# Performance work log

Measured on AMD Instinct MI355X. Metric: run time of the kernel, lower is better.

Reference implementation:

```python
import jax, jax.numpy as jnp
import numpy as np
import math

EMBED = 768
HEADS = 12
DK = EMBED // HEADS
FFN = 3072
NQ = 8
B, S = 4, 2048


def _layernorm(x, g, b, eps=1e-5):
    mu = jnp.mean(x, axis=-1, keepdims=True)
    var = jnp.var(x, axis=-1, keepdims=True)
    return (x - mu) * jax.lax.rsqrt(var + eps) * g + b


def setup_inputs() -> dict:
    key = jax.random.key(0)
    ks = jax.random.split(key, 16)
    std = 0.02
    inp = {
        "x": jax.random.normal(ks[0], (B, S, EMBED), dtype=jnp.float32),
        "mask": jnp.ones((B, S), dtype=jnp.int32),
        # attention projections (torch Linear: W [out, in])
        "wq": jax.random.normal(ks[1], (EMBED, EMBED), jnp.float32) * std,
        "bq": jnp.zeros((EMBED,), jnp.float32),
        "wk": jax.random.normal(ks[2], (EMBED, EMBED), jnp.float32) * std,
        "bk": jnp.zeros((EMBED,), jnp.float32),
        "wv": jax.random.normal(ks[3], (EMBED, EMBED), jnp.float32) * std,
        "bv": jnp.zeros((EMBED,), jnp.float32),
        "wo": jax.random.normal(ks[4], (EMBED, EMBED), jnp.float32) * std,
        "bo": jnp.zeros((EMBED,), jnp.float32),
        # layernorms
        "g1": jnp.ones((EMBED,), jnp.float32),
        "be1": jnp.zeros((EMBED,), jnp.float32),
        "g2": jnp.ones((EMBED,), jnp.float32),
        "be2": jnp.zeros((EMBED,), jnp.float32),
        # quantum FFN: trainable RY angles + two linears
        "theta": jax.random.normal(ks[5], (NQ,), jnp.float32) * 0.1,
        "w1": jax.random.normal(ks[6], (FFN, NQ), jnp.float32) * std,
        "b1": jnp.zeros((FFN,), jnp.float32),
        "w2": jax.random.normal(ks[7], (EMBED, FFN), jnp.float32) * std,
        "b2": jnp.zeros((EMBED,), jnp.float32),
    }
    return inp


def _block(x, mask, wq, bq, wk, bk, wv, bv, wo, bo, g1, be1, g2, be2,
           theta, w1, b1, w2, b2):
    b, s, _ = x.shape
    # --- multi-head attention (dropout = identity at eval) ---
    q = (x @ wq.T + bq).reshape(b, s, HEADS, DK)
    k = (x @ wk.T + bk).reshape(b, s, HEADS, DK)
    v = (x @ wv.T + bv).reshape(b, s, HEADS, DK)
    scores = jnp.einsum("bqhd,bkhd->bhqk", q, k) / math.sqrt(DK)
    scores = jnp.where(mask[:, None, None, :] == 0, -1e9, scores)
    attn = jax.nn.softmax(scores, axis=-1)
    ctx = jnp.einsum("bhqk,bkhd->bqhd", attn, v).reshape(b, s, EMBED)
    attn_out = ctx @ wo.T + bo
    x = _layernorm(x + attn_out, g1, be1)
    # --- quantum FFN: RY(x_i) then RY(theta_i) on |0>, <Z> = cos(x_i+theta_i)
    # (product state, no entanglement -> exact closed form, fully batched)
    meas = jnp.cos(x[..., :NQ] + theta)            # [b, s, NQ]
    h = jax.nn.relu(meas @ w1.T + b1)              # [b, s, FFN]
    ffn_out = h @ w2.T + b2                        # [b, s, EMBED]
    return _layernorm(x + ffn_out, g2, be2)


def reference(x, mask, wq, bq, wk, bk, wv, bv, wo, bo, g1, be1, g2, be2,
              theta, w1, b1, w2, b2):
    return _block(x, mask, wq, bq, wk, bk, wv, bv, wo, bo,
                  g1, be1, g2, be2, theta, w1, b1, w2, b2)
```

## Files before the change

kernel.cpp:

```cpp
#include <hip/hip_runtime.h>
#include <hip/hip_bf16.h>


typedef __bf16 bf16_t;
typedef bf16_t bf16x4 __attribute__((ext_vector_type(4)));
typedef bf16_t bf16x8 __attribute__((ext_vector_type(8)));
typedef float floatx4 __attribute__((ext_vector_type(4)));

#define LOG2E 1.44269504088896f

__device__ __forceinline__ void gload16(const bf16_t* g, bf16_t* l) {
    __builtin_amdgcn_global_load_lds(
        (const __attribute__((address_space(1))) unsigned int*)g,
        (__attribute__((address_space(3))) unsigned int*)l,
        16, 0, 0);
}

__device__ __forceinline__ int swz(int row, int col) {
    return row * 64 + (col ^ ((row & 7) << 3));
}

__global__ __launch_bounds__(256)
void prep(const float* __restrict__ x,
          const float* __restrict__ wq, const float* __restrict__ wk,
          const float* __restrict__ wv, const float* __restrict__ wo,
          const float* __restrict__ w2,
          const float* __restrict__ bq, const float* __restrict__ bk,
          const float* __restrict__ bv,
          bf16_t* __restrict__ xb, bf16_t* __restrict__ wqkv,
          bf16_t* __restrict__ wob, bf16_t* __restrict__ w2b,
          float* __restrict__ bqkv)
{
    const int seg = blockIdx.y;
    const int idx = blockIdx.x * 256 + threadIdx.x;
    if (seg == 0) {
        if (idx >= 1572864) return;
        const float4 f = ((const float4*)x)[idx];
        bf16x4 o = {(bf16_t)f.x, (bf16_t)f.y, (bf16_t)f.z, (bf16_t)f.w};
        ((bf16x4*)xb)[idx] = o;
    } else if (seg == 1) {
        if (idx >= 442368) return;
        const int e = idx * 4;
        float4 f = (e < 589824) ? ((const float4*)wq)[idx]
                 : (e < 1179648) ? ((const float4*)wk)[idx - 147456]
                                 : ((const float4*)wv)[idx - 294912];
        if (e < 589824) { f.x *= 0.125f; f.y *= 0.125f; f.z *= 0.125f; f.w *= 0.125f; }
        bf16x4 o = {(bf16_t)f.x, (bf16_t)f.y, (bf16_t)f.z, (bf16_t)f.w};
        ((bf16x4*)wqkv)[idx] = o;
    } else if (seg == 2) {
        if (idx >= 147456) return;
        const float4 f = ((const float4*)wo)[idx];
        bf16x4 o = {(bf16_t)f.x, (bf16_t)f.y, (bf16_t)f.z, (bf16_t)f.w};
        ((bf16x4*)wob)[idx] = o;
    } else if (seg == 3) {
        if (idx >= 589824) return;
        const float4 f = ((const float4*)w2)[idx];
        bf16x4 o = {(bf16_t)f.x, (bf16_t)f.y, (bf16_t)f.z, (bf16_t)f.w};
        ((bf16x4*)w2b)[idx] = o;
    } else {
        if (idx >= 576) return;
        const int e = idx * 4;
        float4 f = (e < 768) ? ((const float4*)bq)[idx]
                 : (e < 1536) ? ((const float4*)bk)[idx - 192]
                              : ((const float4*)bv)[idx - 384];
        if (e < 768) { f.x *= 0.125f; f.y *= 0.125f; f.z *= 0.125f; f.w *= 0.125f; }
        ((float4*)bqkv)[idx] = f;
    }
}

template<typename TC>
__global__ __launch_bounds__(256)
void gemm_bb(const bf16_t* __restrict__ A, const bf16_t* __restrict__ W,
             const float* __restrict__ bias, TC* __restrict__ C,
             int kPer, int lda, int ldw, int ldc, int splitStride)
{
    __shared__ __align__(16) bf16_t As[2][4096];
    __shared__ __align__(16) bf16_t Bs[2][4096];
    const int tid  = threadIdx.x;
    const int wave = tid >> 6;
    const int lane = tid & 63;
    const int wm = (wave >> 1) * 64;
    const int wn = (wave & 1) * 64;

    const int nwg  = gridDim.x * gridDim.y;
    const int flat = blockIdx.y * gridDim.x + blockIdx.x;
    const int swzb = (flat & 7) * (nwg >> 3) + (flat >> 3);
    const int bm = (swzb / gridDim.x) * 128;
    const int bn = (swzb % gridDim.x) * 128;

    const int fr = lane & 15;
    const int fk = (lane >> 4) * 8;

    const int kBeg = blockIdx.z * kPer;
    const int kEnd = kBeg + kPer;
    C += (size_t)blockIdx.z * splitStride;

    const int srow = tid >> 2;
    const int scol = (tid & 3) * 8;

    floatx4 acc[4][4] = {};

    const bf16_t* gA = A + (size_t)(bm + srow) * lda + scol;
    const bf16_t* gB = W + (size_t)(bn + srow) * ldw + scol;

#define STAGE(buf, kk)                                              \
    {   const bf16_t* ga = gA + (kk);                               \
        const bf16_t* gb = gB + (kk);                               \
        gload16(ga,                    &As[buf][tid * 8]);          \
        gload16(ga + (size_t)64 * lda, &As[buf][tid * 8 + 2048]);   \
        gload16(gb,                    &Bs[buf][tid * 8]);          \
        gload16(gb + (size_t)64 * ldw, &Bs[buf][tid * 8 + 2048]);   \
    }

    STAGE(0, kBeg);
    __syncthreads();

    int cur = 0;
    for (int k0 = kBeg; k0 < kEnd; k0 += 32) {
        if (k0 + 32 < kEnd) STAGE(cur ^ 1, k0 + 32);

        bf16x8 fa[4], fb[4];
        #pragma unroll
        for (int i = 0; i < 4; ++i) {
            fa[i] = *(const bf16x8*)&As[cur][(wm + i * 16 + fr) * 32 + fk];
            fb[i] = *(const bf16x8*)&Bs[cur][(wn + i * 16 + fr) * 32 + fk];
        }
        #pragma unroll
        for (int mi = 0; mi < 4; ++mi)
            #pragma unroll
            for (int ni = 0; ni < 4; ++ni)
                acc[mi][ni] = __builtin_amdgcn_mfma_f32_16x16x32_bf16(
                    fa[mi], fb[ni], acc[mi][ni], 0, 0, 0);

        __syncthreads();
        cur ^= 1;
    }
#undef STAGE

    const int fg = (lane >> 4) * 4;
    const bool addb = (blockIdx.z == 0);
    #pragma unroll
    for (int mi = 0; mi < 4; ++mi) {
        #pragma unroll
        for (int ni = 0; ni < 4; ++ni) {
            const int col = bn + wn + ni * 16 + fr;
            const float bv = addb ? bias[col] : 0.f;
            #pragma unroll
            for (int r = 0; r < 4; ++r) {
                const int row = bm + wm + mi * 16 + fg + r;
                C[(size_t)row * ldc + col] = (TC)(acc[mi][ni][r] + bv);
            }
        }
    }
}

__global__ __launch_bounds__(256)
void attn_mfma(const bf16_t* __restrict__ qkv, const int* __restrict__ mask,
               bf16_t* __restrict__ ctx)
{
    __shared__ __align__(16) bf16_t KsL[2][4096];
    __shared__ __align__(16) bf16_t VtL[2][4096];
    __shared__ __align__(16) bf16_t PlL[4][2048];
    __shared__ float mbL[2][64];

    const int flat = blockIdx.x;
    const int swzb = (flat & 7) * 96 + (flat >> 3);
    const int bh = swzb >> 4;
    const int b = bh / 12, h = bh % 12;
    const int tid  = threadIdx.x;
    const int wave = tid >> 6;
    const int lane = tid & 63;
    const int g    = lane >> 4;
    const int fr   = lane & 15;
    const int qbase = (swzb & 15) * 128 + wave * 32;

    bf16x8 qf[2][2];
    #pragma unroll
    for (int qt = 0; qt < 2; ++qt)
        #pragma unroll
        for (int s = 0; s < 2; ++s) {
            const size_t tok = (size_t)(b * 2048 + qbase + qt * 16 + fr);
            qf[qt][s] = *(const bf16x8*)(qkv + tok * 2304 + h * 64 + s * 32 + g * 8);
        }

    floatx4 o[2][4] = {};
    float lsum[2] = {0.f, 0.f};

    const int skey = tid & 63;
    const int sgrp = tid >> 6;

    bf16x8 rk0, rk1, rv0, rv1;
    float  rmb;
    {
        const size_t ktok = (size_t)(b * 2048 + skey) * 2304 + h * 64;
        rk0 = *(const bf16x8*)(qkv + ktok + 768 + sgrp * 16);
        rk1 = *(const bf16x8*)(qkv + ktok + 768 + sgrp * 16 + 8);
        rv0 = *(const bf16x8*)(qkv + ktok + 1536 + sgrp * 16);
        rv1 = *(const bf16x8*)(qkv + ktok + 1536 + sgrp * 16 + 8);
        rmb = (mask[b * 2048 + skey] == 0) ? -1e9f : 0.f;
    }

    int cur = 0;
    for (int kt = 0; kt < 32; ++kt) {
        *(bf16x8*)&KsL[cur][swz(skey, sgrp * 16)]     = rk0;
        *(bf16x8*)&KsL[cur][swz(skey, sgrp * 16 + 8)] = rk1;
        #pragma unroll
        for (int j = 0; j < 8; ++j) {
            VtL[cur][swz(sgrp * 16 + j,     skey)] = rv0[j];
            VtL[cur][swz(sgrp * 16 + 8 + j, skey)] = rv1[j];
        }
        if (tid < 64) mbL[cur][tid] = rmb;

        if (kt + 1 < 32) {
            const size_t ktok = (size_t)(b * 2048 + (kt + 1) * 64 + skey) * 2304 + h * 64;
            rk0 = *(const bf16x8*)(qkv + ktok + 768 + sgrp * 16);
            rk1 = *(const bf16x8*)(qkv + ktok + 768 + sgrp * 16 + 8);
            rv0 = *(const bf16x8*)(qkv + ktok + 1536 + sgrp * 16);
            rv1 = *(const bf16x8*)(qkv + ktok + 1536 + sgrp * 16 + 8);
            rmb = (mask[b * 2048 + (kt + 1) * 64 + skey] == 0) ? -1e9f : 0.f;
        }

        __syncthreads();

        floatx4 st_[2][4] = {};
        #pragma unroll
        for (int s = 0; s < 2; ++s) {
            bf16x8 kf[4];
            #pragma unroll
            for (int ct = 0; ct < 4; ++ct)
                kf[ct] = *(const bf16x8*)&KsL[cur][swz(ct * 16 + fr, s * 32 + g * 8)];
            #pragma unroll
            for (int qt = 0; qt < 2; ++qt)
                #pragma unroll
                for (int ct = 0; ct < 4; ++ct)
                    st_[qt][ct] = __builtin_amdgcn_mfma_f32_16x16x32_bf16(
                        kf[ct], qf[qt][s], st_[qt][ct], 0, 0, 0);
        }

        #pragma unroll
        for (int qt = 0; qt < 2; ++qt) {
            #pragma unroll
            for (int ct = 0; ct < 4; ++ct) {
                const float4 mb4 = *(const float4*)&mbL[cur][ct * 16 + g * 4];
                const float mbr[4] = { mb4.x, mb4.y, mb4.z, mb4.w };
                bf16x4 pw;
                #pragma unroll
                for (int r = 0; r < 4; ++r) {
                    const float p = __builtin_amdgcn_exp2f(
                        fmaf(st_[qt][ct][r], LOG2E, mbr[r]));
                    lsum[qt] += p;
                    pw[r] = (bf16_t)p;
                }
                *(bf16x4*)&PlL[wave][swz(qt * 16 + fr, ct * 16 + g * 4)] = pw;
            }
        }

        #pragma unroll
        for (int st2 = 0; st2 < 2; ++st2) {
            bf16x8 pf[2];
            #pragma unroll
            for (int qt = 0; qt < 2; ++qt)
                pf[qt] = *(const bf16x8*)&PlL[wave][swz(qt * 16 + fr, st2 * 32 + g * 8)];
            #pragma unroll
            for (int dt = 0; dt < 4; ++dt) {
                const bf16x8 vf = *(const bf16x8*)&VtL[cur][swz(dt * 16 + fr, st2 * 32 + g * 8)];
                #pragma unroll
                for (int qt = 0; qt < 2; ++qt)
                    o[qt][dt] = __builtin_amdgcn_mfma_f32_16x16x32_bf16(
                        pf[qt], vf, o[qt][dt], 0, 0, 0);
            }
        }

        cur ^= 1;
    }

    #pragma unroll
    for (int qt = 0; qt < 2; ++qt) {
        float lf = lsum[qt];
        lf += __shfl_xor(lf, 16, 64);
        lf += __shfl_xor(lf, 32, 64);
        float inv[4];
        #pragma unroll
        for (int r = 0; r < 4; ++r) {
            const float lv = __shfl(lf, (lane & 48) + g * 4 + r, 64);
            inv[r] = 1.f / lv;
        }
        #pragma unroll
        for (int dt = 0; dt < 4; ++dt)
            #pragma unroll
            for (int r = 0; r < 4; ++r) {
                const size_t row = (size_t)(b * 2048 + qbase + qt * 16 + g * 4 + r);
                ctx[row * 768 + h * 64 + dt * 16 + fr] = (bf16_t)(o[qt][dt][r] * inv[r]);
            }
    }
}

__global__ __launch_bounds__(256)
void ln_fuse(const float* __restrict__ xin, const float* __restrict__ proj,
             const float* __restrict__ proj2,
             const float* __restrict__ g, const float* __restrict__ be,
             float* __restrict__ out,
             const float* __restrict__ theta, float* __restrict__ meas)
{
    const int wave = threadIdx.x >> 6;
    const int lane = threadIdx.x & 63;
    const int row  = blockIdx.x * 4 + wave;
    const size_t base = (size_t)row * 768;

    float4 v[3];
    float s1 = 0.f, s2 = 0.f;
    #pragma unroll
    for (int i = 0; i < 3; ++i) {
        const int c4 = lane + i * 64;
        const float4 a  = ((const float4*)(xin  + base))[c4];
        const float4 p  = ((const float4*)(proj + base))[c4];
        const float4 p2 = ((const float4*)(proj2 + base))[c4];
        v[i].x = a.x + p.x + p2.x;
        v[i].y = a.y + p.y + p2.y;
        v[i].z = a.z + p.z + p2.z;
        v[i].w = a.w + p.w + p2.w;
        s1 += v[i].x + v[i].y + v[i].z + v[i].w;
        s2 += v[i].x*v[i].x + v[i].y*v[i].y + v[i].z*v[i].z + v[i].w*v[i].w;
    }
    #pragma unroll
    for (int mk = 32; mk >= 1; mk >>= 1) {
        s1 += __shfl_xor(s1, mk, 64);
        s2 += __shfl_xor(s2, mk, 64);
    }
    const float mu   = s1 * (1.f / 768.f);
    const float var  = s2 * (1.f / 768.f) - mu * mu;
    const float rinv = rsqrtf(var + 1e-5f);

    #pragma unroll
    for (int i = 0; i < 3; ++i) {
        const int c4 = lane + i * 64;
        const float4 gg = ((const float4*)g)[c4];
        const float4 bb = ((const float4*)be)[c4];
        float4 o;
        o.x = (v[i].x - mu) * rinv * gg.x + bb.x;
        o.y = (v[i].y - mu) * rinv * gg.y + bb.y;
        o.z = (v[i].z - mu) * rinv * gg.z + bb.z;
        o.w = (v[i].w - mu) * rinv * gg.w + bb.w;
        ((float4*)(out + base))[c4] = o;
        if (i == 0 && meas != nullptr && lane < 2) {
            meas[row * 8 + lane * 4 + 0] = cosf(o.x + theta[lane * 4 + 0]);
            meas[row * 8 + lane * 4 + 1] = cosf(o.y + theta[lane * 4 + 1]);
            meas[row * 8 + lane * 4 + 2] = cosf(o.z + theta[lane * 4 + 2]);
            meas[row * 8 + lane * 4 + 3] = cosf(o.w + theta[lane * 4 + 3]);
        }
    }
}

__global__ __launch_bounds__(256)
void ffn1(const float* __restrict__ meas, const float* __restrict__ w1,
          const float* __restrict__ b1, bf16_t* __restrict__ h)
{
    const int row = blockIdx.x;
    __shared__ float ms[8];
    if (threadIdx.x < 8) ms[threadIdx.x] = meas[row * 8 + threadIdx.x];
    __syncthreads();
    #pragma unroll
    for (int i = 0; i < 12; ++i) {
        const int f = threadIdx.x + i * 256;
        const float4 wa = *(const float4*)(w1 + f * 8);
        const float4 wb = *(const float4*)(w1 + f * 8 + 4);
        float v = b1[f];
        v += ms[0]*wa.x + ms[1]*wa.y + ms[2]*wa.z + ms[3]*wa.w;
        v += ms[4]*wb.x + ms[5]*wb.y + ms[6]*wb.z + ms[7]*wb.w;
        h[(size_t)row * 3072 + f] = (bf16_t)fmaxf(v, 0.f);
    }
}

extern "C" void kernel_launch(void* const* d_in, const int* in_sizes, int n_in,
                              void* d_out, int out_size, void* d_ws, size_t ws_size,
                              hipStream_t stream)
{
    const float* x     = (const float*)d_in[0];
    const int*   mask  = (const int*)d_in[1];
    const float* wq    = (const float*)d_in[2];
    const float* bq    = (const float*)d_in[3];
    const float* wk    = (const float*)d_in[4];
    const float* bk    = (const float*)d_in[5];
    const float* wv    = (const float*)d_in[6];
    const float* bv    = (const float*)d_in[7];
    const float* wo    = (const float*)d_in[8];
    const float* bo    = (const float*)d_in[9];
    const float* g1    = (const float*)d_in[10];
    const float* be1   = (const float*)d_in[11];
    const float* g2    = (const float*)d_in[12];
    const float* be2   = (const float*)d_in[13];
    const float* theta = (const float*)d_in[14];
    const float* w1    = (const float*)d_in[15];
    const float* b1    = (const float*)d_in[16];
    const float* w2    = (const float*)d_in[17];
    const float* b2    = (const float*)d_in[18];
    float* out = (float*)d_out;

    char* ws = (char*)d_ws;
    bf16_t* qkv    = (bf16_t*)(ws + 0);
    bf16_t* ctx    = (bf16_t*)(ws + 37748736);
    float*  attnp  = (float*)(ws + 50331648);
    float*  y      = (float*)(ws + 100663296);
    float*  meas   = (float*)(ws + 125829120);
    bf16_t* xb     = (bf16_t*)(ws + 126091264);
    bf16_t* wqkv   = (bf16_t*)(ws + 138674176);
    bf16_t* wob    = (bf16_t*)(ws + 142213120);
    bf16_t* w2b    = (bf16_t*)(ws + 143392768);
    float*  bqkv   = (float*)(ws + 148111360);
    float*  ffnp   = (float*)(ws + 0);
    bf16_t* h      = (bf16_t*)(ws + 50331648);

    const dim3 blk(256);

    prep<<<dim3(6144, 5), blk, 0, stream>>>(x, wq, wk, wv, wo, w2, bq, bk, bv,
                                            xb, wqkv, wob, w2b, bqkv);

    gemm_bb<bf16_t><<<dim3(18, 64, 1), blk, 0, stream>>>(
        xb, wqkv, bqkv, qkv, 768, 768, 768, 2304, 0);

    attn_mfma<<<dim3(768), blk, 0, stream>>>(qkv, mask, ctx);

    gemm_bb<float><<<dim3(6, 64, 2), blk, 0, stream>>>(
        ctx, wob, bo, attnp, 384, 768, 768, 768, 6291456);

    ln_fuse<<<dim3(2048), blk, 0, stream>>>(x, attnp, attnp + 6291456,
                                            g1, be1, y, theta, meas);

    ffn1<<<dim3(8192), blk, 0, stream>>>(meas, w1, b1, h);

    gemm_bb<float><<<dim3(6, 64, 2), blk, 0, stream>>>(
        h, w2b, b2, ffnp, 1536, 3072, 3072, 768, 6291456);

    ln_fuse<<<dim3(2048), blk, 0, stream>>>(y, ffnp, ffnp + 6291456,
                                            g2, be2, out, nullptr, nullptr);
}
```

Before: 295.7 us.

## Single-buffer attention K/V LDS and batch four rows per FFN1 block

The attention kernel drops its double-buffered K/V/mask LDS arrays in favour of single buffers with two barriers per key tile. This halves that shared memory to raise occupancy, at the cost of an extra sync per iteration. FFN1 now handles four token rows per block so each w1 weight load is reused across them, and w1 is pre-converted to bf16 in the prep kernel to cut its load bytes. w1 stored as bf16 adds a small rounding difference in the first FFN linear.

```diff
diff --git a/kernel.cpp b/kernel.cpp
--- a/kernel.cpp
+++ b/kernel.cpp
@@ -24,12 +24,12 @@
 void prep(const float* __restrict__ x,
           const float* __restrict__ wq, const float* __restrict__ wk,
           const float* __restrict__ wv, const float* __restrict__ wo,
-          const float* __restrict__ w2,
+          const float* __restrict__ w2, const float* __restrict__ w1,
           const float* __restrict__ bq, const float* __restrict__ bk,
           const float* __restrict__ bv,
           bf16_t* __restrict__ xb, bf16_t* __restrict__ wqkv,
           bf16_t* __restrict__ wob, bf16_t* __restrict__ w2b,
-          float* __restrict__ bqkv)
+          bf16_t* __restrict__ w1b, float* __restrict__ bqkv)
 {
     const int seg = blockIdx.y;
     const int idx = blockIdx.x * 256 + threadIdx.x;
@@ -57,7 +57,7 @@
         const float4 f = ((const float4*)w2)[idx];
         bf16x4 o = {(bf16_t)f.x, (bf16_t)f.y, (bf16_t)f.z, (bf16_t)f.w};
         ((bf16x4*)w2b)[idx] = o;
-    } else {
+    } else if (seg == 4) {
         if (idx >= 576) return;
         const int e = idx * 4;
         float4 f = (e < 768) ? ((const float4*)bq)[idx]
@@ -65,6 +65,11 @@
                               : ((const float4*)bv)[idx - 384];
         if (e < 768) { f.x *= 0.125f; f.y *= 0.125f; f.z *= 0.125f; f.w *= 0.125f; }
         ((float4*)bqkv)[idx] = f;
+    } else {
+        if (idx >= 6144) return;
+        const float4 f = ((const float4*)w1)[idx];
+        bf16x4 o = {(bf16_t)f.x, (bf16_t)f.y, (bf16_t)f.z, (bf16_t)f.w};
+        ((bf16x4*)w1b)[idx] = o;
     }
 }
 
@@ -158,10 +163,10 @@
 void attn_mfma(const bf16_t* __restrict__ qkv, const int* __restrict__ mask,
                bf16_t* __restrict__ ctx)
 {
-    __shared__ __align__(16) bf16_t KsL[2][4096];
-    __shared__ __align__(16) bf16_t VtL[2][4096];
+    __shared__ __align__(16) bf16_t KsL[4096];
+    __shared__ __align__(16) bf16_t VtL[4096];
     __shared__ __align__(16) bf16_t PlL[4][2048];
-    __shared__ float mbL[2][64];
+    __shared__ float mbL[64];
 
     const int flat = blockIdx.x;
     const int swzb = (flat & 7) * 96 + (flat >> 3);
@@ -200,16 +205,17 @@
         rmb = (mask[b * 2048 + skey] == 0) ? -1e9f : 0.f;
     }
 
-    int cur = 0;
     for (int kt = 0; kt < 32; ++kt) {
-        *(bf16x8*)&KsL[cur][swz(skey, sgrp * 16)]     = rk0;
-        *(bf16x8*)&KsL[cur][swz(skey, sgrp * 16 + 8)] = rk1;
+        __syncthreads();
+        *(bf16x8*)&KsL[swz(skey, sgrp * 16)]     = rk0;
+        *(bf16x8*)&KsL[swz(skey, sgrp * 16 + 8)] = rk1;
         #pragma unroll
         for (int j = 0; j < 8; ++j) {
-            VtL[cur][swz(sgrp * 16 + j,     skey)] = rv0[j];
-            VtL[cur][swz(sgrp * 16 + 8 + j, skey)] = rv1[j];
-        }
-        if (tid < 64) mbL[cur][tid] = rmb;
+            VtL[swz(sgrp * 16 + j,     skey)] = rv0[j];
+            VtL[swz(sgrp * 16 + 8 + j, skey)] = rv1[j];
+        }
+        if (tid < 64) mbL[tid] = rmb;
+        __syncthreads();
 
         if (kt + 1 < 32) {
             const size_t ktok = (size_t)(b * 2048 + (kt + 1) * 64 + skey) * 2304 + h * 64;
@@ -220,15 +226,13 @@
             rmb = (mask[b * 2048 + (kt + 1) * 64 + skey] == 0) ? -1e9f : 0.f;
         }
 
-        __syncthreads();
-
         floatx4 st_[2][4] = {};
         #pragma unroll
         for (int s = 0; s < 2; ++s) {
             bf16x8 kf[4];
             #pragma unroll
             for (int ct = 0; ct < 4; ++ct)
-                kf[ct] = *(const bf16x8*)&KsL[cur][swz(ct * 16 + fr, s * 32 + g * 8)];
+                kf[ct] = *(const bf16x8*)&KsL[swz(ct * 16 + fr, s * 32 + g * 8)];
             #pragma unroll
             for (int qt = 0; qt < 2; ++qt)
                 #pragma unroll
@@ -241,7 +245,7 @@
         for (int qt = 0; qt < 2; ++qt) {
             #pragma unroll
             for (int ct = 0; ct < 4; ++ct) {
-                const float4 mb4 = *(const float4*)&mbL[cur][ct * 16 + g * 4];
+                const float4 mb4 = *(const float4*)&mbL[ct * 16 + g * 4];
                 const float mbr[4] = { mb4.x, mb4.y, mb4.z, mb4.w };
                 bf16x4 pw;
                 #pragma unroll
@@ -263,15 +267,13 @@
                 pf[qt] = *(const bf16x8*)&PlL[wave][swz(qt * 16 + fr, st2 * 32 + g * 8)];
             #pragma unroll
             for (int dt = 0; dt < 4; ++dt) {
-                const bf16x8 vf = *(const bf16x8*)&VtL[cur][swz(dt * 16 + fr, st2 * 32 + g * 8)];
+                const bf16x8 vf = *(const bf16x8*)&VtL[swz(dt * 16 + fr, st2 * 32 + g * 8)];
                 #pragma unroll
                 for (int qt = 0; qt < 2; ++qt)
                     o[qt][dt] = __builtin_amdgcn_mfma_f32_16x16x32_bf16(
                         pf[qt], vf, o[qt][dt], 0, 0, 0);
             }
         }
-
-        cur ^= 1;
     }
 
     #pragma unroll
@@ -352,22 +354,29 @@
 }
 
 __global__ __launch_bounds__(256)
-void ffn1(const float* __restrict__ meas, const float* __restrict__ w1,
+void ffn1(const float* __restrict__ meas, const bf16_t* __restrict__ w1b,
           const float* __restrict__ b1, bf16_t* __restrict__ h)
 {
-    const int row = blockIdx.x;
-    __shared__ float ms[8];
-    if (threadIdx.x < 8) ms[threadIdx.x] = meas[row * 8 + threadIdx.x];
+    const int row0 = blockIdx.x * 4;
+    __shared__ float ms[4][8];
+    if (threadIdx.x < 32)
+        ms[threadIdx.x >> 3][threadIdx.x & 7] = meas[row0 * 8 + threadIdx.x];
     __syncthreads();
     #pragma unroll
     for (int i = 0; i < 12; ++i) {
         const int f = threadIdx.x + i * 256;
-        const float4 wa = *(const float4*)(w1 + f * 8);
-        const float4 wb = *(const float4*)(w1 + f * 8 + 4);
-        float v = b1[f];
-        v += ms[0]*wa.x + ms[1]*wa.y + ms[2]*wa.z + ms[3]*wa.w;
-        v += ms[4]*wb.x + ms[5]*wb.y + ms[6]*wb.z + ms[7]*wb.w;
-        h[(size_t)row * 3072 + f] = (bf16_t)fmaxf(v, 0.f);
+        const bf16x8 w = *(const bf16x8*)(w1b + f * 8);
+        float wv[8];
+        #pragma unroll
+        for (int j = 0; j < 8; ++j) wv[j] = (float)w[j];
+        const float bias = b1[f];
+        #pragma unroll
+        for (int r = 0; r < 4; ++r) {
+            float v = bias;
+            #pragma unroll
+            for (int j = 0; j < 8; ++j) v += ms[r][j] * wv[j];
+            h[(size_t)(row0 + r) * 3072 + f] = (bf16_t)fmaxf(v, 0.f);
+        }
     }
 }
 
@@ -407,13 +416,14 @@
     bf16_t* wob    = (bf16_t*)(ws + 142213120);
     bf16_t* w2b    = (bf16_t*)(ws + 143392768);
     float*  bqkv   = (float*)(ws + 148111360);
+    bf16_t* w1b    = (bf16_t*)(ws + 148120576);
     float*  ffnp   = (float*)(ws + 0);
     bf16_t* h      = (bf16_t*)(ws + 50331648);
 
     const dim3 blk(256);
 
-    prep<<<dim3(6144, 5), blk, 0, stream>>>(x, wq, wk, wv, wo, w2, bq, bk, bv,
-                                            xb, wqkv, wob, w2b, bqkv);
+    prep<<<dim3(6144, 6), blk, 0, stream>>>(x, wq, wk, wv, wo, w2, w1, bq, bk, bv,
+                                            xb, wqkv, wob, w2b, w1b, bqkv);
 
     gemm_bb<bf16_t><<<dim3(18, 64, 1), blk, 0, stream>>>(
         xb, wqkv, bqkv, qkv, 768, 768, 768, 2304, 0);
@@ -426,7 +436,7 @@
     ln_fuse<<<dim3(2048), blk, 0, stream>>>(x, attnp, attnp + 6291456,
                                             g1, be1, y, theta, meas);
 
-    ffn1<<<dim3(8192), blk, 0, stream>>>(meas, w1, b1, h);
+    ffn1<<<dim3(2048), blk, 0, stream>>>(meas, w1b, b1, h);
 
     gemm_bb<float><<<dim3(6, 64, 2), blk, 0, stream>>>(
         h, w2b, b2, ffnp, 1536, 3072, 3072, 768, 6291456);
```

Result: no change. 292.0 us (-1.3%).
